# Kernel optimization log

Measured on AMD Instinct MI355X. Metric: run time of the kernel, lower is better.

The kernel has to match this reference:

```python
import jax, jax.numpy as jnp
import numpy as np

N_POS = 8192          # number of positive samples
N_NEG = 4000          # negatives per positive
N_TOT = N_POS + N_POS * N_NEG


def setup_inputs() -> dict:
    key = jax.random.key(0)
    k1, k2 = jax.random.split(key)
    predict_val = jax.random.normal(k1, (N_TOT,), dtype=jnp.float32)
    # 'index' is a permutation; the module reorders predict_val by argsort(index)
    index = jax.random.permutation(k2, jnp.arange(N_TOT, dtype=jnp.int64))
    return {"predict_val": predict_val, "index": index, "num": N_NEG, "num_pos": N_POS}


def reference(predict_val, index, num, num_pos):
    # index_tuple = sorted(enumerate(index)) by value -> reorder by argsort(index)
    pv = predict_val[jnp.argsort(index)]
    pos = pv[:num_pos]                                  # [num_pos]
    neg = pv[num_pos:num_pos + num_pos * num]
    neg = neg.reshape(num_pos, num)                     # [num_pos, num]
    # rank of pos among {neg, pos} sorted descending == 1 + #(neg > pos)
    # (ties are randomly broken in the original; measure-zero for continuous scores)
    rank = 1 + jnp.sum(neg > pos[:, None], axis=-1)     # [num_pos], int
    sample_mrr = 1.0 / rank.astype(pv.dtype)            # [num_pos]
    mrr = jnp.mean(sample_mrr)
    return mrr, sample_mrr
```

## Files before the change

### kernel.cpp

```cpp
#include <hip/hip_runtime.h>


constexpr int N_POS = 8192;
constexpr int N_NEG = 4000;
constexpr int NSLOT = N_POS / 4;

typedef int   vint4   __attribute__((ext_vector_type(4)));
typedef float vfloat4 __attribute__((ext_vector_type(4)));
typedef unsigned int u32;
typedef unsigned long long u64;

__global__ __launch_bounds__(256) void scatter_pos_kernel(
    const vint4* __restrict__ idx4, const float* __restrict__ pv,
    float* __restrict__ pos, u64* __restrict__ cnt, int nvec) {
  const int gtid = blockIdx.x * 256 + threadIdx.x;
  if (gtid < NSLOT) cnt[gtid] = 0ull;
  const int stride = gridDim.x * 256;
  int j = gtid;
#define SC_ELEM(V, JJ)                                   \
  if ((V).x < N_POS) pos[(V).x] = pv[4 * (JJ) + 0];      \
  if ((V).y < N_POS) pos[(V).y] = pv[4 * (JJ) + 1];      \
  if ((V).z < N_POS) pos[(V).z] = pv[4 * (JJ) + 2];      \
  if ((V).w < N_POS) pos[(V).w] = pv[4 * (JJ) + 3];
  for (; j + stride < nvec; j += 2 * stride) {
    vint4 a = idx4[j];
    vint4 b = idx4[j + stride];
    SC_ELEM(a, j)
    SC_ELEM(b, j + stride)
  }
  for (; j < nvec; j += stride) {
    vint4 a = idx4[j];
    SC_ELEM(a, j)
  }
#undef SC_ELEM
}

__global__ __launch_bounds__(1024) void count_kernel(
    const vint4* __restrict__ idx4, const vfloat4* __restrict__ pv4,
    const float* __restrict__ pos, u64* __restrict__ cnt, int nvec) {
  __shared__ float pos_lds[N_POS];
  __shared__ u32   lcnt[N_POS];
  for (int i = threadIdx.x; i < N_POS; i += 1024) {
    pos_lds[i] = pos[i];
    lcnt[i] = 0u;
  }
  __syncthreads();

  const int stride = gridDim.x * 1024;
  int j = blockIdx.x * 1024 + threadIdx.x;
#define CT_ELEM(IV, XV)                                              \
  if ((IV) >= N_POS) {                                               \
    unsigned r = (unsigned)((IV) - N_POS) / (unsigned)N_NEG;         \
    if ((XV) > pos_lds[r]) atomicAdd(&lcnt[r], 1u);                  \
  }
#define CT_VEC(V, X)                                                 \
  CT_ELEM((V).x, (X).x) CT_ELEM((V).y, (X).y)                        \
  CT_ELEM((V).z, (X).z) CT_ELEM((V).w, (X).w)
  for (; j + stride < nvec; j += 2 * stride) {
    vint4 va = idx4[j];
    vint4 vb = idx4[j + stride];
    vfloat4 xa = __builtin_nontemporal_load(&pv4[j]);
    vfloat4 xb = __builtin_nontemporal_load(&pv4[j + stride]);
    CT_VEC(va, xa)
    CT_VEC(vb, xb)
  }
  for (; j < nvec; j += stride) {
    vint4 va = idx4[j];
    vfloat4 xa = __builtin_nontemporal_load(&pv4[j]);
    CT_VEC(va, xa)
  }
#undef CT_VEC
#undef CT_ELEM
  __syncthreads();

  for (int s = threadIdx.x; s < NSLOT; s += 1024) {
    u32 c0 = lcnt[4 * s + 0], c1 = lcnt[4 * s + 1];
    u32 c2 = lcnt[4 * s + 2], c3 = lcnt[4 * s + 3];
    u64 p = (u64)c0 | ((u64)c1 << 16) | ((u64)c2 << 32) | ((u64)c3 << 48);
    if (p) atomicAdd(&cnt[s], p);
  }
}

__global__ __launch_bounds__(1024) void finalize_kernel(
    const u64* __restrict__ cnt, float* __restrict__ out) {
  __shared__ float wsum[16];
  int t = threadIdx.x;
  float lsum = 0.f;
  for (int s = t; s < NSLOT; s += 1024) {
    u64 p = cnt[s];
    float m0 = 1.0f / (float)(1u + (u32)(p & 0xFFFFu));
    float m1 = 1.0f / (float)(1u + (u32)((p >> 16) & 0xFFFFu));
    float m2 = 1.0f / (float)(1u + (u32)((p >> 32) & 0xFFFFu));
    float m3 = 1.0f / (float)(1u + (u32)((p >> 48) & 0xFFFFu));
    vfloat4 m = {m0, m1, m2, m3};
    *(vfloat4*)&out[1 + 4 * s] = m;
    lsum += m0 + m1 + m2 + m3;
  }
#pragma unroll
  for (int off = 32; off > 0; off >>= 1) lsum += __shfl_down(lsum, off, 64);
  if ((t & 63) == 0) wsum[t >> 6] = lsum;
  __syncthreads();
  if (t == 0) {
    float tot = 0.f;
#pragma unroll
    for (int w = 0; w < 16; ++w) tot += wsum[w];
    out[0] = tot / (float)N_POS;
  }
}

extern "C" void kernel_launch(void* const* d_in, const int* in_sizes, int n_in,
                              void* d_out, int out_size, void* d_ws, size_t ws_size,
                              hipStream_t stream) {
  const float* pv = (const float*)d_in[0];
  const int* idx = (const int*)d_in[1];
  float* out = (float*)d_out;
  float* pos = (float*)d_ws;
  u64* cnt = (u64*)((char*)d_ws + 32 * 1024);
  int nvec = in_sizes[0] / 4;

  scatter_pos_kernel<<<2048, 256, 0, stream>>>((const vint4*)idx, pv, pos,
                                               cnt, nvec);
  count_kernel<<<512, 1024, 0, stream>>>((const vint4*)idx, (const vfloat4*)pv,
                                         pos, cnt, nvec);
  finalize_kernel<<<1, 1024, 0, stream>>>(cnt, out);
}
```

Measured before the change: 289.1 us.

## Fuse finalize into count kernel via last-block detection; unroll loads by four

```diff
diff --git a/kernel.cpp b/kernel.cpp
--- a/kernel.cpp
+++ b/kernel.cpp
@@ -4,6 +4,7 @@
 constexpr int N_POS = 8192;
 constexpr int N_NEG = 4000;
 constexpr int NSLOT = N_POS / 4;
+constexpr int CNT_BLOCKS = 512;
 
 typedef int   vint4   __attribute__((ext_vector_type(4)));
 typedef float vfloat4 __attribute__((ext_vector_type(4)));
@@ -14,7 +15,7 @@
     const vint4* __restrict__ idx4, const float* __restrict__ pv,
     float* __restrict__ pos, u64* __restrict__ cnt, int nvec) {
   const int gtid = blockIdx.x * 256 + threadIdx.x;
-  if (gtid < NSLOT) cnt[gtid] = 0ull;
+  if (gtid <= NSLOT) cnt[gtid] = 0ull;
   const int stride = gridDim.x * 256;
   int j = gtid;
 #define SC_ELEM(V, JJ)                                   \
@@ -22,11 +23,15 @@
   if ((V).y < N_POS) pos[(V).y] = pv[4 * (JJ) + 1];      \
   if ((V).z < N_POS) pos[(V).z] = pv[4 * (JJ) + 2];      \
   if ((V).w < N_POS) pos[(V).w] = pv[4 * (JJ) + 3];
-  for (; j + stride < nvec; j += 2 * stride) {
+  for (; j + 3 * stride < nvec; j += 4 * stride) {
     vint4 a = idx4[j];
     vint4 b = idx4[j + stride];
+    vint4 c = idx4[j + 2 * stride];
+    vint4 d = idx4[j + 3 * stride];
     SC_ELEM(a, j)
     SC_ELEM(b, j + stride)
+    SC_ELEM(c, j + 2 * stride)
+    SC_ELEM(d, j + 3 * stride)
   }
   for (; j < nvec; j += stride) {
     vint4 a = idx4[j];
@@ -37,9 +42,12 @@
 
 __global__ __launch_bounds__(1024) void count_kernel(
     const vint4* __restrict__ idx4, const vfloat4* __restrict__ pv4,
-    const float* __restrict__ pos, u64* __restrict__ cnt, int nvec) {
+    const float* __restrict__ pos, u64* __restrict__ cnt,
+    float* __restrict__ out, int nvec) {
   __shared__ float pos_lds[N_POS];
   __shared__ u32   lcnt[N_POS];
+  __shared__ float wsum[16];
+  __shared__ int is_last;
   for (int i = threadIdx.x; i < N_POS; i += 1024) {
     pos_lds[i] = pos[i];
     lcnt[i] = 0u;
@@ -56,13 +64,19 @@
 #define CT_VEC(V, X)                                                 \
   CT_ELEM((V).x, (X).x) CT_ELEM((V).y, (X).y)                        \
   CT_ELEM((V).z, (X).z) CT_ELEM((V).w, (X).w)
-  for (; j + stride < nvec; j += 2 * stride) {
+  for (; j + 3 * stride < nvec; j += 4 * stride) {
     vint4 va = idx4[j];
     vint4 vb = idx4[j + stride];
+    vint4 vc = idx4[j + 2 * stride];
+    vint4 vd = idx4[j + 3 * stride];
     vfloat4 xa = __builtin_nontemporal_load(&pv4[j]);
     vfloat4 xb = __builtin_nontemporal_load(&pv4[j + stride]);
+    vfloat4 xc = __builtin_nontemporal_load(&pv4[j + 2 * stride]);
+    vfloat4 xd = __builtin_nontemporal_load(&pv4[j + 3 * stride]);
     CT_VEC(va, xa)
     CT_VEC(vb, xb)
+    CT_VEC(vc, xc)
+    CT_VEC(vd, xd)
   }
   for (; j < nvec; j += stride) {
     vint4 va = idx4[j];
@@ -79,15 +93,20 @@
     u64 p = (u64)c0 | ((u64)c1 << 16) | ((u64)c2 << 32) | ((u64)c3 << 48);
     if (p) atomicAdd(&cnt[s], p);
   }
-}
 
-__global__ __launch_bounds__(1024) void finalize_kernel(
-    const u64* __restrict__ cnt, float* __restrict__ out) {
-  __shared__ float wsum[16];
-  int t = threadIdx.x;
+  __threadfence();
+  if (threadIdx.x == 0) {
+    u64 prev = atomicAdd(&cnt[NSLOT], 1ull);
+    is_last = (prev == (u64)(gridDim.x - 1));
+  }
+  __syncthreads();
+  if (!is_last) return;
+  __threadfence();
+
   float lsum = 0.f;
-  for (int s = t; s < NSLOT; s += 1024) {
-    u64 p = cnt[s];
+  for (int s = threadIdx.x; s < NSLOT; s += 1024) {
+    u64 p = __hip_atomic_load(&cnt[s], __ATOMIC_RELAXED,
+                              __HIP_MEMORY_SCOPE_AGENT);
     float m0 = 1.0f / (float)(1u + (u32)(p & 0xFFFFu));
     float m1 = 1.0f / (float)(1u + (u32)((p >> 16) & 0xFFFFu));
     float m2 = 1.0f / (float)(1u + (u32)((p >> 32) & 0xFFFFu));
@@ -98,9 +117,9 @@
   }
 #pragma unroll
   for (int off = 32; off > 0; off >>= 1) lsum += __shfl_down(lsum, off, 64);
-  if ((t & 63) == 0) wsum[t >> 6] = lsum;
+  if ((threadIdx.x & 63) == 0) wsum[threadIdx.x >> 6] = lsum;
   __syncthreads();
-  if (t == 0) {
+  if (threadIdx.x == 0) {
     float tot = 0.f;
 #pragma unroll
     for (int w = 0; w < 16; ++w) tot += wsum[w];
@@ -120,7 +139,7 @@
 
   scatter_pos_kernel<<<2048, 256, 0, stream>>>((const vint4*)idx, pv, pos,
                                                cnt, nvec);
-  count_kernel<<<512, 1024, 0, stream>>>((const vint4*)idx, (const vfloat4*)pv,
-                                         pos, cnt, nvec);
-  finalize_kernel<<<1, 1024, 0, stream>>>(cnt, out);
+  count_kernel<<<CNT_BLOCKS, 1024, 0, stream>>>((const vint4*)idx,
+                                                (const vfloat4*)pv, pos, cnt,
+                                                out, nvec);
 }
```

Result: slower. 447.2 us (+54.7%).
